# Kernel optimization log

Measured on AMD Instinct MI355X. Metric: run time of the kernel, lower is better.

## Reference

```python
import jax, jax.numpy as jnp
import numpy as np

N_TOKEN = 267735
D = 512           # d_embed == d_proj
DIV = 4
CUTS = [0, 20000, 40000, 200000, 267735]  # cutoff_ends
N_TOKENS_BATCH = 1024  # len*bsz


def setup_inputs() -> dict:
    key = jax.random.key(0)
    ks = jax.random.split(key, 16)
    inp = {}
    inp["hidden"] = jax.random.normal(ks[0], (N_TOKENS_BATCH, D), jnp.float32)
    inp["target"] = jax.random.randint(ks[1], (N_TOKENS_BATCH,), 0, N_TOKEN)
    d_embs = [D // DIV ** i for i in range(4)]          # 512, 128, 32, 8
    sizes = [CUTS[i + 1] - CUTS[i] for i in range(4)]   # 20000, 20000, 160000, 67735
    for i in range(4):
        inp[f"W{i}"] = jax.random.normal(ks[2 + 3 * i], (sizes[i], d_embs[i]), jnp.float32) * (d_embs[i] ** -0.5)
        inp[f"b{i}"] = jax.random.normal(ks[3 + 3 * i], (sizes[i],), jnp.float32) * 0.01
        inp[f"proj{i}"] = jax.random.normal(ks[4 + 3 * i], (D, d_embs[i]), jnp.float32) * (D ** -0.5)
    inp["cluster_weight"] = jax.random.normal(ks[14], (3, D), jnp.float32) * (D ** -0.5)
    inp["cluster_bias"] = jax.random.normal(ks[15], (3,), jnp.float32) * 0.01
    return inp


def reference(hidden, target, W0, b0, proj0, W1, b1, proj1, W2, b2, proj2, W3, b3, proj3, cluster_weight, cluster_bias):
    n = jnp.arange(target.shape[0])
    # head = shortlist vocab + one logit per tail cluster
    head_w = jnp.concatenate([W0, cluster_weight], axis=0)   # [20003, D]
    head_b = jnp.concatenate([b0, cluster_bias], axis=0)     # [20003]
    head_logit = (hidden @ proj0) @ head_w.T + head_b        # einsum('bd,de,ev->bv')
    head_lp = jax.nn.log_softmax(head_logit, axis=-1)        # [N, 20003]
    head_size = head_lp.shape[1]
    # cluster id per token (0 = shortlist, 1..3 = tails)
    cid = ((target >= CUTS[1]).astype(jnp.int32)
           + (target >= CUTS[2]).astype(jnp.int32)
           + (target >= CUTS[3]).astype(jnp.int32))
    # shortlist: nll = -head_logprob[n, target]
    nll = -head_lp[n, jnp.clip(target, 0, CUTS[1] - 1)]
    for i, (Wi, bi, pi) in enumerate([(W1, b1, proj1), (W2, b2, proj2), (W3, b3, proj3)], start=1):
        l, r = CUTS[i], CUTS[i + 1]
        tail_lp = jax.nn.log_softmax((hidden @ pi) @ Wi.T + bi, axis=-1)  # [N, r-l]
        rel = jnp.clip(target - l, 0, r - l - 1)
        # faithful to original: head column indexed as head_logprob[:, -i]
        lp_i = head_lp[:, head_size - i] + tail_lp[n, rel]
        nll = jnp.where(cid == i, -lp_i, nll)
    return nll
```

## Files before the change

kernel.cpp:

```cpp
#include <hip/hip_runtime.h>

typedef short s16x8 __attribute__((ext_vector_type(8)));
typedef unsigned short u16x8 __attribute__((ext_vector_type(8)));
typedef float f32x4 __attribute__((ext_vector_type(4)));
typedef unsigned short ushort;

#define NTOK 1024
#define DHID 512

#define VH   20003
#define KH   512
#define VH_PAD 20480

#define V1   20000
#define K1   128
#define V1_PAD 20480

#define V2   160000
#define K2   32
#define V2_PAD 163840
#define TPC_2 80

#define V3   67735
#define K3   32
#define V3_PAD 68608
#define TPC_3 64

#define NCHK_H 320
#define NCHK_1 320
#define NCHK_2 128
#define NCHK_3 67

#define PAD_BIAS (-1e30f)
#define LOG2E 1.4426950408889634f
#define LN2F  0.6931471805599453f

#define PIPE_BARRIER() do {                                   \
        asm volatile("s_barrier" ::: "memory");               \
        __builtin_amdgcn_sched_barrier(0);                    \
    } while (0)

#define OFF_HW   0UL
#define OFF_W1   (OFF_HW  + (unsigned long)VH_PAD*KH*2)
#define OFF_W2   (OFF_W1  + (unsigned long)V1_PAD*K1*2)
#define OFF_W3   (OFF_W2  + (unsigned long)V2_PAD*K2*2)
#define OFF_HID  (OFF_W3  + (unsigned long)V3_PAD*K3*2)
#define OFF_PT0  (OFF_HID + (unsigned long)NTOK*DHID*2)
#define OFF_PT1  (OFF_PT0 + (unsigned long)512*DHID*2)
#define OFF_PT2  (OFF_PT1 + (unsigned long)128*DHID*2)
#define OFF_PT3  (OFF_PT2 + (unsigned long)32*DHID*2)
#define OFF_H0   (OFF_PT3 + (unsigned long)32*DHID*2)
#define OFF_H1   (OFF_H0  + (unsigned long)NTOK*512*2)
#define OFF_H2   (OFF_H1  + (unsigned long)NTOK*128*2)
#define OFF_H3   (OFF_H2  + (unsigned long)NTOK*32*2)
#define OFF_HB   (OFF_H3  + (unsigned long)NTOK*32*2)
#define OFF_B1   (OFF_HB  + (unsigned long)VH_PAD*4)
#define OFF_B2   (OFF_B1  + (unsigned long)V1_PAD*4)
#define OFF_B3   (OFF_B2  + (unsigned long)V2_PAD*4)
#define OFF_SH   (OFF_B3  + (unsigned long)V3_PAD*4)
#define OFF_S1   (OFF_SH  + (unsigned long)NTOK*NCHK_H*4)
#define OFF_S2   (OFF_S1  + (unsigned long)NTOK*NCHK_1*4)
#define OFF_S3   (OFF_S2  + (unsigned long)NTOK*NCHK_2*4)

__device__ __forceinline__ ushort f2bf(float f) {
    union { float f; unsigned u; } x; x.f = f;
    unsigned r = x.u + 0x7fffu + ((x.u >> 16) & 1u);
    return (ushort)(r >> 16);
}
__device__ __forceinline__ float bf2f(ushort h) {
    union { unsigned u; float f; } x; x.u = ((unsigned)h) << 16;
    return x.f;
}
__device__ __forceinline__ f32x4 mfma_bf16(s16x8 a, s16x8 b, f32x4 c) {
    return __builtin_amdgcn_mfma_f32_16x16x32_bf16(a, b, c, 0, 0, 0);
}
__device__ __forceinline__ void ld8(const float* p, float* v) {
    float4 a = *(const float4*)p, b = *(const float4*)(p + 4);
    v[0]=a.x; v[1]=a.y; v[2]=a.z; v[3]=a.w; v[4]=b.x; v[5]=b.y; v[6]=b.z; v[7]=b.w;
}
__device__ __forceinline__ void gld_lds16(const ushort* g, ushort* l) {
    __builtin_amdgcn_global_load_lds(
        (const __attribute__((address_space(1))) unsigned int*)g,
        (__attribute__((address_space(3))) unsigned int*)l, 16, 0, 0);
}

#define WB_HW  20480L
#define WB_W1  5120L
#define WB_W2  10240L
#define WB_W3  4288L
#define WB_HID 1024L
#define WB_PT0 512L
#define WB_PT1 128L
#define WB_PT2 32L
#define WB_PT3 32L
#define WB_TOTAL (WB_HW+WB_W1+WB_W2+WB_W3+WB_HID+WB_PT0+WB_PT1+WB_PT2+WB_PT3)

__global__ __launch_bounds__(256) void prep_wswz(
    const float* __restrict__ hidden,
    const float* __restrict__ W0, const float* __restrict__ cw,
    const float* __restrict__ W1, const float* __restrict__ W2, const float* __restrict__ W3,
    const float* __restrict__ p0, const float* __restrict__ p1,
    const float* __restrict__ p2, const float* __restrict__ p3,
    ushort* __restrict__ hw, ushort* __restrict__ ow1,
    ushort* __restrict__ ow2, ushort* __restrict__ ow3,
    ushort* __restrict__ hid,
    ushort* __restrict__ pT0, ushort* __restrict__ pT1,
    ushort* __restrict__ pT2, ushort* __restrict__ pT3)
{
    int lane = threadIdx.x & 63;
    int r = lane & 15, quad = lane >> 4;
    long wb0 = (long)blockIdx.x * 4 + (threadIdx.x >> 6);
    long nw = (long)gridDim.x * 4;
    for (long wb = wb0; wb < WB_TOTAL; wb += nw) {
        long b = wb;
        float vals[8];
        #pragma unroll
        for (int j = 0; j < 8; ++j) vals[j] = 0.f;
        float scale = LOG2E;
        ushort* dst;
        if (b < WB_HW) {
            long tile = b >> 4, ks = b & 15;
            long v = tile * 16 + r, k = ks * 32 + quad * 8;
            if (v < 20000)      ld8(W0 + v * 512 + k, vals);
            else if (v < VH)    ld8(cw + (v - 20000) * 512 + k, vals);
            dst = hw + b * 512 + (long)lane * 8;
        } else if ((b -= WB_HW) < WB_W1) {
            long tile = b >> 2, ks = b & 3;
            long v = tile * 16 + r, k = ks * 32 + quad * 8;
            if (v < V1) ld8(W1 + v * 128 + k, vals);
            dst = ow1 + b * 512 + (long)lane * 8;
        } else if ((b -= WB_W1) < WB_W2) {
            long v = b * 16 + r;
            if (v < V2) ld8(W2 + v * 32 + quad * 8, vals);
            dst = ow2 + b * 512 + (long)lane * 8;
        } else if ((b -= WB_W2) < WB_W3) {
            long v = b * 16 + r;
            if (v < V3 && quad == 0) ld8(W3 + v * 8, vals);
            dst = ow3 + b * 512 + (long)lane * 8;
        } else if ((b -= WB_W3) < WB_HID) {
            scale = 1.f;
            long tile = b >> 4, ks = b & 15;
            long v = tile * 16 + r, k = ks * 32 + quad * 8;
            ld8(hidden + v * 512 + k, vals);
            dst = hid + b * 512 + (long)lane * 8;
        } else if ((b -= WB_HID) < WB_PT0) {
            scale = 1.f;
            long tile = b >> 4, ks = b & 15;
            long c = tile * 16 + r, k = ks * 32 + quad * 8;
            #pragma unroll
            for (int j = 0; j < 8; ++j) vals[j] = p0[(k + j) * 512 + c];
            dst = pT0 + b * 512 + (long)lane * 8;
        } else if ((b -= WB_PT0) < WB_PT1) {
            scale = 1.f;
            long tile = b >> 4, ks = b & 15;
            long c = tile * 16 + r, k = ks * 32 + quad * 8;
            #pragma unroll
            for (int j = 0; j < 8; ++j) vals[j] = p1[(k + j) * 128 + c];
            dst = pT1 + b * 512 + (long)lane * 8;
        } else if ((b -= WB_PT1) < WB_PT2) {
            scale = 1.f;
            long tile = b >> 4, ks = b & 15;
            long c = tile * 16 + r, k = ks * 32 + quad * 8;
            #pragma unroll
            for (int j = 0; j < 8; ++j) vals[j] = p2[(k + j) * 32 + c];
            dst = pT2 + b * 512 + (long)lane * 8;
        } else {
            scale = 1.f;
            b -= WB_PT2;
            long tile = b >> 4, ks = b & 15;
            long c = tile * 16 + r, k = ks * 32 + quad * 8;
            if (c < 8) {
                #pragma unroll
                for (int j = 0; j < 8; ++j) vals[j] = p3[(k + j) * 8 + c];
            }
            dst = pT3 + b * 512 + (long)lane * 8;
        }
        u16x8 o;
        #pragma unroll
        for (int j = 0; j < 8; ++j) o[j] = f2bf(vals[j] * scale);
        *(u16x8*)dst = o;
    }
}

#define E_HB  ((long)VH_PAD)
#define E_B1  ((long)V1_PAD)
#define E_B2  ((long)V2_PAD)
#define E_B3  ((long)V3_PAD)
#define E_BIAS (E_HB+E_B1+E_B2+E_B3)

__global__ __launch_bounds__(256) void prep_bias(
    const float* __restrict__ b0, const float* __restrict__ b1,
    const float* __restrict__ b2, const float* __restrict__ b3,
    const float* __restrict__ cb,
    float* __restrict__ hbp, float* __restrict__ ob1,
    float* __restrict__ ob2, float* __restrict__ ob3)
{
    long stride = (long)gridDim.x * blockDim.x;
    for (long i = (long)blockIdx.x * blockDim.x + threadIdx.x; i < E_BIAS; i += stride) {
        long j = i;
        if (j < E_HB) {
            hbp[j] = ((j < 20000) ? b0[j] : (j < VH) ? cb[j - 20000] : PAD_BIAS) * LOG2E;
        } else if ((j -= E_HB) < E_B1) {
            ob1[j] = ((j < V1) ? b1[j] : PAD_BIAS) * LOG2E;
        } else if ((j -= E_B1) < E_B2) {
            ob2[j] = ((j < V2) ? b2[j] : PAD_BIAS) * LOG2E;
        } else { j -= E_B2;
            ob3[j] = ((j < V3) ? b3[j] : PAD_BIAS) * LOG2E;
        }
    }
}

__device__ __forceinline__ void gemm_body(
    const ushort* __restrict__ A, const ushort* __restrict__ Bt,
    ushort* __restrict__ Hout, int dpad, int c_tile)
{
    int wave = threadIdx.x >> 6, lane = threadIdx.x & 63;
    int quad = lane >> 4, colid = lane & 15;
    int m_tile = blockIdx.x * 4 + wave;
    const ushort* Ab = A + ((long)m_tile * 16) * 512 + lane * 8;
    const ushort* Bb = Bt + ((long)c_tile * 16) * 512 + lane * 8;
    f32x4 acc = {0.f, 0.f, 0.f, 0.f};
    #pragma unroll
    for (int ks = 0; ks < 16; ++ks) {
        s16x8 a = *(const s16x8*)(Ab + ks * 512);
        s16x8 b = *(const s16x8*)(Bb + ks * 512);
        acc = mfma_bf16(a, b, acc);
    }
    int KBo = dpad >> 5;
    int col = c_tile * 16 + colid;
    int ks_o = col >> 5, q_o = (col >> 3) & 3, j_o = col & 7;
    #pragma unroll
    for (int r = 0; r < 4; ++r) {
        int rm = quad * 4 + r;
        Hout[((long)m_tile * KBo + ks_o) * 512 + (q_o * 16 + rm) * 8 + j_o] = f2bf(acc[r]);
    }
}

__global__ __launch_bounds__(256) void gemm_all(
    const ushort* __restrict__ hid,
    const ushort* __restrict__ pT0, const ushort* __restrict__ pT1,
    const ushort* __restrict__ pT2, const ushort* __restrict__ pT3,
    ushort* __restrict__ H0, ushort* __restrict__ H1,
    ushort* __restrict__ H2, ushort* __restrict__ H3)
{
    int y = blockIdx.y;
    if (y < 32)      gemm_body(hid, pT0, H0, 512, y);
    else if (y < 40) gemm_body(hid, pT1, H1, 128, y - 32);
    else if (y < 42) gemm_body(hid, pT2, H2, 32,  y - 40);
    else             gemm_body(hid, pT3, H3, 32,  y - 42);
}

template<int KB>
__global__ __launch_bounds__(256, 2) void gemm_lse_k(
    const ushort* __restrict__ A, const ushort* __restrict__ W,
    const float* __restrict__ biasp, float* __restrict__ part_s,
    int n_chunks)
{
    __shared__ __align__(16) ushort lds[3 * 16 * 512];
    int bid = blockIdx.x;
    int k = bid & 7, j = bid >> 3;
    int nb = k * 20 + (j >> 3);
    int mb = j & 7;
    int wave = threadIdx.x >> 6, lane = threadIdx.x & 63;
    int wr = wave >> 1, wc = wave & 1;
    int quad = lane >> 4, colid = lane & 15;

    f32x4 acc[4][4];
    #pragma unroll
    for (int mi = 0; mi < 4; ++mi)
        #pragma unroll
        for (int ni = 0; ni < 4; ++ni) acc[mi][ni] = (f32x4){0.f, 0.f, 0.f, 0.f};

    const long Abase = (long)mb * 8, Wbase = (long)nb * 8;

#define STAGE_K(ks, bf) do {                                                     \
        ushort* d_ = lds + (bf) * (16 * 512);                                    \
        _Pragma("unroll")                                                        \
        for (int i_ = 0; i_ < 2; ++i_) {                                         \
            int t_ = 2 * wave + i_;                                              \
            gld_lds16(A + ((Abase + t_) * KB + (ks)) * 512 + lane * 8,           \
                      d_ + t_ * 512 + lane * 8);                                 \
            gld_lds16(W + ((Wbase + t_) * KB + (ks)) * 512 + lane * 8,           \
                      d_ + (8 + t_) * 512 + lane * 8);                           \
        }                                                                        \
    } while (0)

#define COMP_K(bf) do {                                                          \
        const ushort* b_ = lds + (bf) * (16 * 512);                              \
        s16x8 bfg[4];                                                            \
        _Pragma("unroll")                                                        \
        for (int ni = 0; ni < 4; ++ni)                                           \
            bfg[ni] = *(const s16x8*)(b_ + (8 + wc * 4 + ni) * 512 + lane * 8);  \
        _Pragma("unroll")                                                        \
        for (int mi = 0; mi < 4; ++mi) {                                         \
            s16x8 af = *(const s16x8*)(b_ + (wr * 4 + mi) * 512 + lane * 8);     \
            _Pragma("unroll")                                                    \
            for (int ni = 0; ni < 4; ++ni)                                       \
                acc[mi][ni] = mfma_bf16(af, bfg[ni], acc[mi][ni]);               \
        }                                                                        \
    } while (0)

    STAGE_K(0, 0);
    STAGE_K(1, 1);
    for (int g = 0; g < KB - 1; ++g) {
        asm volatile("s_waitcnt vmcnt(4)" ::: "memory");
        PIPE_BARRIER();
        if (g + 2 < KB) STAGE_K(g + 2, (g + 2) % 3);
        COMP_K(g % 3);
        asm volatile("s_waitcnt lgkmcnt(0)" ::: "memory");
        __builtin_amdgcn_sched_barrier(0);
    }
    asm volatile("s_waitcnt vmcnt(0)" ::: "memory");
    PIPE_BARRIER();
    COMP_K((KB - 1) % 3);
#undef STAGE_K
#undef COMP_K

    float bv[4];
    long c0 = (long)nb * 128 + wc * 64 + colid;
    #pragma unroll
    for (int ni = 0; ni < 4; ++ni) bv[ni] = biasp[c0 + ni * 16];
    int chunk = nb * 2 + wc;
    #pragma unroll
    for (int mi = 0; mi < 4; ++mi) {
        #pragma unroll
        for (int r = 0; r < 4; ++r) {
            float v = 0.f;
            #pragma unroll
            for (int ni = 0; ni < 4; ++ni)
                v += __builtin_amdgcn_exp2f(acc[mi][ni][r] + bv[ni]);
            v += __shfl_xor(v, 1);
            v += __shfl_xor(v, 2);
            v += __shfl_xor(v, 4);
            v += __shfl_xor(v, 8);
            if (colid == 0) {
                int m = mb * 128 + wr * 64 + mi * 16 + quad * 4 + r;
                part_s[(long)m * n_chunks + chunk] = v;
            }
        }
    }
}

template<int U>
__global__ __launch_bounds__(256) void fused_lse_direct(
    const ushort* __restrict__ A, const ushort* __restrict__ W,
    const float* __restrict__ biasp, float* __restrict__ part_s,
    int tpc, int n_chunks, int cpx)
{
    int bid = blockIdx.x;
    int k = bid & 7, j = bid >> 3;
    int chunk = k * cpx + (j >> 4);
    int mblk = j & 15;
    if (chunk >= n_chunks) return;
    int wave = threadIdx.x >> 6, lane = threadIdx.x & 63;
    int quad = lane >> 4, colid = lane & 15;
    int m_tile = mblk * 4 + wave;
    long t0 = (long)chunk * tpc;

    s16x8 afrag = *(const s16x8*)(A + (long)m_tile * 512 + lane * 8);
    const ushort* Wc = W + t0 * 512;
    const float* bch = biasp + t0 * 16;

    float s_acc[4] = {0.f, 0.f, 0.f, 0.f};
    for (int vt = 0; vt < tpc; vt += U) {
        f32x4 acc[U];
        #pragma unroll
        for (int u = 0; u < U; ++u) {
            float bv = bch[(vt + u) * 16 + colid];
            acc[u] = (f32x4){bv, bv, bv, bv};
        }
        #pragma unroll
        for (int u = 0; u < U; ++u) {
            s16x8 b = *(const s16x8*)(Wc + (long)(vt + u) * 512 + lane * 8);
            acc[u] = mfma_bf16(afrag, b, acc[u]);
        }
        #pragma unroll
        for (int u = 0; u < U; ++u)
            #pragma unroll
            for (int r = 0; r < 4; ++r)
                s_acc[r] += __builtin_amdgcn_exp2f(acc[u][r]);
    }
    #pragma unroll
    for (int r = 0; r < 4; ++r) {
        float v = s_acc[r];
        v += __shfl_xor(v, 1);
        v += __shfl_xor(v, 2);
        v += __shfl_xor(v, 4);
        v += __shfl_xor(v, 8);
        if (colid == 0) {
            int m = m_tile * 16 + quad * 4 + r;
            part_s[(long)m * n_chunks + chunk] = v;
        }
    }
}

__device__ __forceinline__ float swz_dot(const ushort* __restrict__ H, int m,
                                         const ushort* __restrict__ Wm, long vrow,
                                         int K, int lane)
{
    float d = 0.f;
    if (lane * 8 < K) {
        int ks = lane >> 2, q = lane & 3;
        int KB = K >> 5;
        const ushort* hp = H + ((long)(m >> 4) * KB + ks) * 512 + (q * 16 + (m & 15)) * 8;
        const ushort* wp = Wm + ((vrow >> 4) * KB + ks) * 512 + (q * 16 + (int)(vrow & 15)) * 8;
        #pragma unroll
        for (int j = 0; j < 8; ++j) d += bf2f(hp[j]) * bf2f(wp[j]);
    }
    d += __shfl_xor(d, 1);  d += __shfl_xor(d, 2);  d += __shfl_xor(d, 4);
    d += __shfl_xor(d, 8);  d += __shfl_xor(d, 16); d += __shfl_xor(d, 32);
    return d;
}

__global__ __launch_bounds__(256) void finalize_kernel(
    const int* __restrict__ target,
    const ushort* __restrict__ H0, const ushort* __restrict__ hw,
    const float* __restrict__ hbp, const float* __restrict__ sH,
    const ushort* __restrict__ H1, const ushort* __restrict__ w1,
    const float* __restrict__ b1p, const float* __restrict__ s1,
    const ushort* __restrict__ H2, const ushort* __restrict__ w2,
    const float* __restrict__ b2p, const float* __restrict__ s2,
    const ushort* __restrict__ H3, const ushort* __restrict__ w3,
    const float* __restrict__ b3p, const float* __restrict__ s3,
    float* __restrict__ out)
{
    int wave = threadIdx.x >> 6, lane = threadIdx.x & 63;
    int m = blockIdx.x * 4 + wave;
    int t = target[m];
    int cid = (t >= 20000) + (t >= 40000) + (t >= 200000);

    float s = 0.f;
    for (int i = lane; i < NCHK_H; i += 64) s += sH[(long)m * NCHK_H + i];
    s += __shfl_xor(s, 1);  s += __shfl_xor(s, 2);  s += __shfl_xor(s, 4);
    s += __shfl_xor(s, 8);  s += __shfl_xor(s, 16); s += __shfl_xor(s, 32);
    float lse_h = __logf(s);

    int hc = (cid == 0) ? t : (20003 - cid);
    float d = swz_dot(H0, m, hw, hc, 512, lane);
    float nll = lse_h - (d + hbp[hc]) * LN2F;

    if (cid > 0) {
        const ushort *Hi, *Wi; const float *bi, *si; int K, nc, l;
        if (cid == 1)      { Hi = H1; Wi = w1; bi = b1p; si = s1; K = 128; nc = NCHK_1; l = 20000; }
        else if (cid == 2) { Hi = H2; Wi = w2; bi = b2p; si = s2; K = 32;  nc = NCHK_2; l = 40000; }
        else               { Hi = H3; Wi = w3; bi = b3p; si = s3; K = 32;  nc = NCHK_3; l = 200000; }
        int rel = t - l;
        float ts = 0.f;
        for (int i = lane; i < nc; i += 64) ts += si[(long)m * nc + i];
        ts += __shfl_xor(ts, 1);  ts += __shfl_xor(ts, 2);  ts += __shfl_xor(ts, 4);
        ts += __shfl_xor(ts, 8);  ts += __shfl_xor(ts, 16); ts += __shfl_xor(ts, 32);
        float lse_t = __logf(ts);
        float dt = swz_dot(Hi, m, Wi, rel, K, lane);
        nll += lse_t - (dt + bi[rel]) * LN2F;
    }
    if (lane == 0) out[m] = nll;
}

extern "C" void kernel_launch(void* const* d_in, const int* in_sizes, int n_in,
                              void* d_out, int out_size, void* d_ws, size_t ws_size,
                              hipStream_t stream) {
    const float* hidden = (const float*)d_in[0];
    const int*   target = (const int*)d_in[1];
    const float* W0 = (const float*)d_in[2];
    const float* b0 = (const float*)d_in[3];
    const float* p0 = (const float*)d_in[4];
    const float* W1 = (const float*)d_in[5];
    const float* b1 = (const float*)d_in[6];
    const float* p1 = (const float*)d_in[7];
    const float* W2 = (const float*)d_in[8];
    const float* b2 = (const float*)d_in[9];
    const float* p2 = (const float*)d_in[10];
    const float* W3 = (const float*)d_in[11];
    const float* b3 = (const float*)d_in[12];
    const float* p3 = (const float*)d_in[13];
    const float* cw = (const float*)d_in[14];
    const float* cb = (const float*)d_in[15];

    char* ws = (char*)d_ws;
    ushort* hw  = (ushort*)(ws + OFF_HW);
    ushort* ow1 = (ushort*)(ws + OFF_W1);
    ushort* ow2 = (ushort*)(ws + OFF_W2);
    ushort* ow3 = (ushort*)(ws + OFF_W3);
    ushort* hid = (ushort*)(ws + OFF_HID);
    ushort* pT0 = (ushort*)(ws + OFF_PT0);
    ushort* pT1 = (ushort*)(ws + OFF_PT1);
    ushort* pT2 = (ushort*)(ws + OFF_PT2);
    ushort* pT3 = (ushort*)(ws + OFF_PT3);
    ushort* H0  = (ushort*)(ws + OFF_H0);
    ushort* H1  = (ushort*)(ws + OFF_H1);
    ushort* H2  = (ushort*)(ws + OFF_H2);
    ushort* H3  = (ushort*)(ws + OFF_H3);
    float* hbp = (float*)(ws + OFF_HB);
    float* b1p = (float*)(ws + OFF_B1);
    float* b2p = (float*)(ws + OFF_B2);
    float* b3p = (float*)(ws + OFF_B3);
    float* sH  = (float*)(ws + OFF_SH);
    float* s1  = (float*)(ws + OFF_S1);
    float* s2  = (float*)(ws + OFF_S2);
    float* s3  = (float*)(ws + OFF_S3);

    prep_wswz<<<10464, 256, 0, stream>>>(hidden, W0, cw, W1, W2, W3,
                                         p0, p1, p2, p3,
                                         hw, ow1, ow2, ow3, hid, pT0, pT1, pT2, pT3);
    prep_bias<<<1072, 256, 0, stream>>>(b0, b1, b2, b3, cb, hbp, b1p, b2p, b3p);

    gemm_all<<<dim3(NTOK / 64, 44), 256, 0, stream>>>(hid, pT0, pT1, pT2, pT3,
                                                      H0, H1, H2, H3);

    gemm_lse_k<16><<<1280, 256, 0, stream>>>(H0, hw, hbp, sH, NCHK_H);
    gemm_lse_k<4><<<1280, 256, 0, stream>>>(H1, ow1, b1p, s1, NCHK_1);
    fused_lse_direct<8><<<2048, 256, 0, stream>>>(H2, ow2, b2p, s2, TPC_2, NCHK_2, 16);
    fused_lse_direct<8><<<1152, 256, 0, stream>>>(H3, ow3, b3p, s3, TPC_3, NCHK_3, 9);

    finalize_kernel<<<NTOK / 4, 256, 0, stream>>>(target,
        H0, hw, hbp, sH, H1, ow1, b1p, s1, H2, ow2, b2p, s2, H3, ow3, b3p, s3,
        (float*)d_out);
}
```

Baseline: 231.3 us.

## Halve GEMM-LSE N-tile for higher occupancy and merge tail-2/3 LSE launches

The head and tail-1 GEMM+exp-sum kernels now use a 128x64 output tile instead of 128x128. This cuts accumulator registers and LDS so three blocks fit per CU, and doubles the number of blocks and partial-sum chunks. The two fused_lse_direct launches for tails 2 and 3 are merged into one grid that branches on block index, removing a kernel launch and letting the two workloads share the device. In exchange, each block reuses its A operand across fewer columns, there are more partial sums for finalize to reduce, and the staging loop now has a select between A and W sources.

```diff
diff --git a/kernel.cpp b/kernel.cpp
--- a/kernel.cpp
+++ b/kernel.cpp
@@ -26,8 +26,8 @@
 #define V3_PAD 68608
 #define TPC_3 64
 
-#define NCHK_H 320
-#define NCHK_1 320
+#define NCHK_H 640
+#define NCHK_1 640
 #define NCHK_2 128
 #define NCHK_3 67
 
@@ -251,51 +251,52 @@
 }
 
 template<int KB>
-__global__ __launch_bounds__(256, 2) void gemm_lse_k(
+__global__ __launch_bounds__(256, 3) void gemm_lse_k(
     const ushort* __restrict__ A, const ushort* __restrict__ W,
     const float* __restrict__ biasp, float* __restrict__ part_s,
     int n_chunks)
 {
-    __shared__ __align__(16) ushort lds[3 * 16 * 512];
+    __shared__ __align__(16) ushort lds[3 * 12 * 512];
     int bid = blockIdx.x;
     int k = bid & 7, j = bid >> 3;
-    int nb = k * 20 + (j >> 3);
+    int nb = k * 40 + (j >> 3);
     int mb = j & 7;
     int wave = threadIdx.x >> 6, lane = threadIdx.x & 63;
     int wr = wave >> 1, wc = wave & 1;
     int quad = lane >> 4, colid = lane & 15;
 
-    f32x4 acc[4][4];
+    f32x4 acc[4][2];
     #pragma unroll
     for (int mi = 0; mi < 4; ++mi)
         #pragma unroll
-        for (int ni = 0; ni < 4; ++ni) acc[mi][ni] = (f32x4){0.f, 0.f, 0.f, 0.f};
-
-    const long Abase = (long)mb * 8, Wbase = (long)nb * 8;
+        for (int ni = 0; ni < 2; ++ni) acc[mi][ni] = (f32x4){0.f, 0.f, 0.f, 0.f};
+
+    const long Abase = (long)mb * 8;
+    const long Wbase = (long)nb * 4;
 
 #define STAGE_K(ks, bf) do {                                                     \
-        ushort* d_ = lds + (bf) * (16 * 512);                                    \
+        ushort* d_ = lds + (bf) * (12 * 512);                                    \
         _Pragma("unroll")                                                        \
-        for (int i_ = 0; i_ < 2; ++i_) {                                         \
-            int t_ = 2 * wave + i_;                                              \
-            gld_lds16(A + ((Abase + t_) * KB + (ks)) * 512 + lane * 8,           \
-                      d_ + t_ * 512 + lane * 8);                                 \
-            gld_lds16(W + ((Wbase + t_) * KB + (ks)) * 512 + lane * 8,           \
-                      d_ + (8 + t_) * 512 + lane * 8);                           \
+        for (int i_ = 0; i_ < 3; ++i_) {                                         \
+            int t_ = 3 * wave + i_;                                              \
+            const ushort* s_ = (t_ < 8)                                          \
+                ? A + ((Abase + t_) * KB + (ks)) * 512 + lane * 8                \
+                : W + ((Wbase + (t_ - 8)) * KB + (ks)) * 512 + lane * 8;         \
+            gld_lds16(s_, d_ + t_ * 512 + lane * 8);                             \
         }                                                                        \
     } while (0)
 
 #define COMP_K(bf) do {                                                          \
-        const ushort* b_ = lds + (bf) * (16 * 512);                              \
-        s16x8 bfg[4];                                                            \
+        const ushort* b_ = lds + (bf) * (12 * 512);                              \
+        s16x8 bfg[2];                                                            \
         _Pragma("unroll")                                                        \
-        for (int ni = 0; ni < 4; ++ni)                                           \
-            bfg[ni] = *(const s16x8*)(b_ + (8 + wc * 4 + ni) * 512 + lane * 8);  \
+        for (int ni = 0; ni < 2; ++ni)                                           \
+            bfg[ni] = *(const s16x8*)(b_ + (8 + wc * 2 + ni) * 512 + lane * 8);  \
         _Pragma("unroll")                                                        \
         for (int mi = 0; mi < 4; ++mi) {                                         \
             s16x8 af = *(const s16x8*)(b_ + (wr * 4 + mi) * 512 + lane * 8);     \
             _Pragma("unroll")                                                    \
-            for (int ni = 0; ni < 4; ++ni)                                       \
+            for (int ni = 0; ni < 2; ++ni)                                       \
                 acc[mi][ni] = mfma_bf16(af, bfg[ni], acc[mi][ni]);               \
         }                                                                        \
     } while (0)
@@ -303,7 +304,7 @@
     STAGE_K(0, 0);
     STAGE_K(1, 1);
     for (int g = 0; g < KB - 1; ++g) {
-        asm volatile("s_waitcnt vmcnt(4)" ::: "memory");
+        asm volatile("s_waitcnt vmcnt(3)" ::: "memory");
         PIPE_BARRIER();
         if (g + 2 < KB) STAGE_K(g + 2, (g + 2) % 3);
         COMP_K(g % 3);
@@ -316,19 +317,17 @@
 #undef STAGE_K
 #undef COMP_K
 
-    float bv[4];
-    long c0 = (long)nb * 128 + wc * 64 + colid;
+    float bv[2];
+    long c0 = (long)nb * 64 + wc * 32 + colid;
     #pragma unroll
-    for (int ni = 0; ni < 4; ++ni) bv[ni] = biasp[c0 + ni * 16];
+    for (int ni = 0; ni < 2; ++ni) bv[ni] = biasp[c0 + ni * 16];
     int chunk = nb * 2 + wc;
     #pragma unroll
     for (int mi = 0; mi < 4; ++mi) {
         #pragma unroll
         for (int r = 0; r < 4; ++r) {
-            float v = 0.f;
-            #pragma unroll
-            for (int ni = 0; ni < 4; ++ni)
-                v += __builtin_amdgcn_exp2f(acc[mi][ni][r] + bv[ni]);
+            float v = __builtin_amdgcn_exp2f(acc[mi][0][r] + bv[0])
+                    + __builtin_amdgcn_exp2f(acc[mi][1][r] + bv[1]);
             v += __shfl_xor(v, 1);
             v += __shfl_xor(v, 2);
             v += __shfl_xor(v, 4);
@@ -343,12 +342,19 @@
 
 template<int U>
 __global__ __launch_bounds__(256) void fused_lse_direct(
-    const ushort* __restrict__ A, const ushort* __restrict__ W,
-    const float* __restrict__ biasp, float* __restrict__ part_s,
-    int tpc, int n_chunks, int cpx)
+    const ushort* __restrict__ A2, const ushort* __restrict__ W2p,
+    const float* __restrict__ b2p, float* __restrict__ s2,
+    const ushort* __restrict__ A3, const ushort* __restrict__ W3p,
+    const float* __restrict__ b3p, float* __restrict__ s3)
 {
     int bid = blockIdx.x;
-    int k = bid & 7, j = bid >> 3;
+    const ushort *A, *W; const float* biasp; float* part_s;
+    int tpc, n_chunks, cpx, lb;
+    if (bid < 2048) { A = A2; W = W2p; biasp = b2p; part_s = s2;
+                      tpc = TPC_2; n_chunks = NCHK_2; cpx = 16; lb = bid; }
+    else            { A = A3; W = W3p; biasp = b3p; part_s = s3;
+                      tpc = TPC_3; n_chunks = NCHK_3; cpx = 9; lb = bid - 2048; }
+    int k = lb & 7, j = lb >> 3;
     int chunk = k * cpx + (j >> 4);
     int mblk = j & 15;
     if (chunk >= n_chunks) return;
@@ -507,10 +513,10 @@
     gemm_all<<<dim3(NTOK / 64, 44), 256, 0, stream>>>(hid, pT0, pT1, pT2, pT3,
                                                       H0, H1, H2, H3);
 
-    gemm_lse_k<16><<<1280, 256, 0, stream>>>(H0, hw, hbp, sH, NCHK_H);
-    gemm_lse_k<4><<<1280, 256, 0, stream>>>(H1, ow1, b1p, s1, NCHK_1);
-    fused_lse_direct<8><<<2048, 256, 0, stream>>>(H2, ow2, b2p, s2, TPC_2, NCHK_2, 16);
-    fused_lse_direct<8><<<1152, 256, 0, stream>>>(H3, ow3, b3p, s3, TPC_3, NCHK_3, 9);
+    gemm_lse_k<16><<<2560, 256, 0, stream>>>(H0, hw, hbp, sH, NCHK_H);
+    gemm_lse_k<4><<<2560, 256, 0, stream>>>(H1, ow1, b1p, s1, NCHK_1);
+    fused_lse_direct<8><<<3200, 256, 0, stream>>>(H2, ow2, b2p, s2,
+                                                  H3, ow3, b3p, s3);
 
     finalize_kernel<<<NTOK / 4, 256, 0, stream>>>(target,
         H0, hw, hbp, sH, H1, ow1, b1p, s1, H2, ow2, b2p, s2, H3, ow3, b3p, s3,
```

After: 240.0 us. 1.04x slower.
